# Kernel tuning notes

Hardware: AMD Instinct MI355X
Metric: run time of the kernel (lower is better)

The kernel has to match this reference:

```python
import jax, jax.numpy as jnp
import numpy as np

B, S, D = 4, 2048, 1024
NH, NKV = 16, 4
HD = D // NH  # 64


def _rope(x, freqs):
    # x: [B, H, S, HD], freqs: [B, S, HD//2]
    cos = jnp.concatenate([jnp.cos(freqs), jnp.cos(freqs)], axis=-1)[:, None]  # [B,1,S,HD]
    sin = jnp.concatenate([jnp.sin(freqs), jnp.sin(freqs)], axis=-1)[:, None]
    x1, x2 = x[..., : HD // 2], x[..., HD // 2:]
    rot = jnp.concatenate([-x2, x1], axis=-1)
    return x * cos + rot * sin


def setup_inputs() -> dict:
    key = jax.random.key(0)
    ks = jax.random.split(key, 9)
    return {
        "hidden_states": jax.random.normal(ks[0], (B, S, D), jnp.float32),
        "rotary_pos_emb": jax.random.normal(ks[1], (B, S, HD // 2), jnp.float32),
        "Wq": jax.random.normal(ks[2], (D, NH * HD), jnp.float32) * 0.02,
        "bq": jax.random.normal(ks[3], (NH * HD,), jnp.float32) * 0.02,
        "Wk": jax.random.normal(ks[4], (D, NKV * HD), jnp.float32) * 0.02,
        "bk": jax.random.normal(ks[5], (NKV * HD,), jnp.float32) * 0.02,
        "Wv": jax.random.normal(ks[6], (D, NKV * HD), jnp.float32) * 0.02,
        "bv": jax.random.normal(ks[7], (NKV * HD,), jnp.float32) * 0.02,
        "Wo": jax.random.normal(ks[8], (NH * HD, D), jnp.float32) * 0.02,
    }


def reference(hidden_states, rotary_pos_emb, Wq, bq, Wk, bk, Wv, bv, Wo):
    b, s, _ = hidden_states.shape
    # projections -> [B, H, S, HD]
    q = (hidden_states @ Wq + bq).reshape(b, s, NH, HD).transpose(0, 2, 1, 3)
    k = (hidden_states @ Wk + bk).reshape(b, s, NKV, HD).transpose(0, 2, 1, 3)
    v = (hidden_states @ Wv + bv).reshape(b, s, NKV, HD).transpose(0, 2, 1, 3)
    q = _rope(q, rotary_pos_emb)
    k = _rope(k, rotary_pos_emb)
    groups = NH // NKV
    k = jnp.repeat(k, groups, axis=1)  # [B, NH, S, HD]
    v = jnp.repeat(v, groups, axis=1)
    scaling = HD ** -0.5
    scores = jnp.einsum("bhqd,bhkd->bhqk", q, k) * scaling
    probs = jax.nn.softmax(scores.astype(jnp.float32), axis=-1).astype(q.dtype)
    out = jnp.einsum("bhqk,bhkd->bhqd", probs, v)
    out = out.transpose(0, 2, 1, 3).reshape(b, s, NH * HD)
    return out @ Wo
```

## Files before the change

kernel.cpp:

```cpp
#include <hip/hip_runtime.h>
#include <hip/hip_bf16.h>

#define BB 4
#define SS 2048
#define DD 1024
#define NH 16
#define NKV 4
#define HD 64
#define MROWS (BB*SS)
#define NQKV (NH*HD + 2*NKV*HD)
#define KOFF (NH*HD)

typedef short v8s __attribute__((ext_vector_type(8)));
typedef short v4s __attribute__((ext_vector_type(4)));
typedef float v4f __attribute__((ext_vector_type(4)));
typedef unsigned short u16;
typedef unsigned int u32;

__device__ __forceinline__ float bf2f(u16 u){
  union { float f; u32 i; } x; x.i = ((u32)u) << 16; return x.f;
}
__device__ __forceinline__ u16 f2bf(float f){
  union { __hip_bfloat16 h; u16 u; } x; x.h = __float2bfloat16(f); return x.u;
}
__device__ __forceinline__ u32 cvtpk(float lo, float hi){
  u32 r;
  asm("v_cvt_pk_bf16_f32 %0, %1, %2" : "=v"(r) : "v"(lo), "v"(hi));
  return r;
}
__device__ __forceinline__ float fmax3(float a, float b, float c){
  return fmaxf(fmaxf(a, b), c);
}
__device__ __forceinline__ void gl_lds16(const u16* g, u16* l){
  __builtin_amdgcn_global_load_lds(
      (const __attribute__((address_space(1))) u32*)g,
      (__attribute__((address_space(3))) u32*)l, 16, 0, 0);
}


__global__ void cast_x(const float* __restrict__ in, u16* __restrict__ out, int n4){
  int i = blockIdx.x*256 + threadIdx.x;
  if (i >= n4) return;
  float4 v = reinterpret_cast<const float4*>(in)[i];
  ushort4 o;
  o.x = f2bf(v.x); o.y = f2bf(v.y); o.z = f2bf(v.z); o.w = f2bf(v.w);
  reinterpret_cast<ushort4*>(out)[i] = o;
}

__global__ void build_bqkv(const float* __restrict__ Wq, const float* __restrict__ Wk,
                           const float* __restrict__ Wv, const float* __restrict__ bq,
                           const float* __restrict__ bk, const float* __restrict__ bv,
                           u16* __restrict__ Bt, float* __restrict__ bias){
  int idx = blockIdx.x*256 + threadIdx.x;
  int n = idx >> 10, k = idx & 1023;
  float v;
  if (n < 1024)      v = Wq[k*1024 + n];
  else if (n < 1280) v = Wk[k*256 + (n-1024)];
  else               v = Wv[k*256 + (n-1280)];
  Bt[idx] = f2bf(v);
  if (k == 0) bias[n] = (n < 1024) ? bq[n] : (n < 1280 ? bk[n-1024] : bv[n-1280]);
}

__global__ void build_wo(const float* __restrict__ Wo, u16* __restrict__ Bt){
  int idx = blockIdx.x*256 + threadIdx.x;
  int n = idx >> 10, k = idx & 1023;
  Bt[idx] = f2bf(Wo[k*1024 + n]);
}

__global__ void build_trig(const float* __restrict__ fr, float2* __restrict__ trig){
  int i = blockIdx.x*256 + threadIdx.x;
  float f = fr[i];
  float sn, cs; __sincosf(f, &sn, &cs);
  trig[i] = make_float2(cs, sn);
}

__global__ void rope_k(u16* __restrict__ QKV, const float* __restrict__ fr){
  int idx = blockIdx.x*256 + threadIdx.x;
  int d  = idx & 31;
  int hh = (idx >> 5) & 3;
  long row = idx >> 7;
  int col = KOFF + hh*HD + d;
  u16* p = QKV + row*NQKV;
  float x1 = bf2f(p[col]);
  float x2 = bf2f(p[col+32]);
  float f = fr[row*32 + d];
  float sn, cs; __sincosf(f, &sn, &cs);
  p[col]    = f2bf(x1*cs - x2*sn);
  p[col+32] = f2bf(x2*cs + x1*sn);
}


template<bool BIAS, typename OT>
__global__ __launch_bounds__(256) void gemm_bt(
    const u16* __restrict__ A, const u16* __restrict__ Bt,
    const float* __restrict__ bias, OT* __restrict__ C,
    int K, int ldc)
{
  __shared__ u16 As[128*32];
  __shared__ u16 Bs[128*32];
  const int tid = threadIdx.x;
  const int wid = tid >> 6, lane = tid & 63;
  const int g = lane >> 4, c = lane & 15;
  const long brow = (long)blockIdx.y * 128;
  const long bcol = (long)blockIdx.x * 128;
  const int wr = (wid >> 1) * 64, wc = (wid & 1) * 64;
  const int srow = tid >> 2;
  const int scol = (tid & 3) * 8;
  const u16* ga = &A [(brow + srow)*K + scol];
  const u16* gb = &Bt[(bcol + srow)*K + scol];
  u16* la = &As[(wid*64)*8];
  u16* lb = &Bs[(wid*64)*8];
  v4f acc[4][4] = {};
  for (int kt = 0; kt < K; kt += 32) {
    __syncthreads();
    gl_lds16(ga + kt,          la);
    gl_lds16(ga + 64*K + kt,   la + 256*8);
    gl_lds16(gb + kt,          lb);
    gl_lds16(gb + 64*K + kt,   lb + 256*8);
    __syncthreads();
    v8s af[4], bf[4];
    #pragma unroll
    for (int m=0;m<4;m++) af[m] = *reinterpret_cast<const v8s*>(&As[(wr + m*16 + c)*32 + g*8]);
    #pragma unroll
    for (int n=0;n<4;n++) bf[n] = *reinterpret_cast<const v8s*>(&Bs[(wc + n*16 + c)*32 + g*8]);
    __builtin_amdgcn_s_setprio(1);
    #pragma unroll
    for (int m=0;m<4;m++)
      #pragma unroll
      for (int n=0;n<4;n++)
        acc[m][n] = __builtin_amdgcn_mfma_f32_16x16x32_bf16(af[m], bf[n], acc[m][n], 0,0,0);
    __builtin_amdgcn_s_setprio(0);
  }
  #pragma unroll
  for (int m=0;m<4;m++)
    #pragma unroll
    for (int n=0;n<4;n++) {
      int col = (int)bcol + wc + n*16 + c;
      float badd = BIAS ? bias[col] : 0.0f;
      #pragma unroll
      for (int r2=0;r2<4;r2++){
        long row = brow + wr + m*16 + g*4 + r2;
        float v = acc[m][n][r2] + badd;
        if constexpr (sizeof(OT)==2) C[row*ldc + col] = (OT)f2bf(v);
        else                         C[row*ldc + col] = (OT)v;
      }
    }
}


__global__ __launch_bounds__(512) void attn_k(const u16* __restrict__ QKV,
                                              const float2* __restrict__ trig,
                                              u16* __restrict__ Out){
  __shared__ u16 Ks[2][64][72];
  __shared__ u16 Vs[2][64][72];
  const int tid = threadIdx.x;
  const int wid = tid >> 6, lane = tid & 63;
  const int g = lane >> 4, c = lane & 15;
  const int qt = blockIdx.x & 7;
  const int bh = blockIdx.x >> 3;
  const int b = bh >> 4, h = bh & 15;
  const int kvh = h >> 2;
  const u16* Qb = QKV + (long)b*SS*NQKV + h*HD;
  const u16* Kb = QKV + (long)b*SS*NQKV + KOFF + kvh*HD;
  const u16* Vb = Kb + NKV*HD;

  const float SCL = 0.125f * 1.44269504088896f;
  v8s qf[2][2];
  #pragma unroll
  for (int qn=0;qn<2;qn++){
    int lrow = qt*256 + wid*32 + qn*16 + c;
    v8s q0 = *reinterpret_cast<const v8s*>(&Qb[(long)lrow*NQKV + g*8]);
    v8s q1 = *reinterpret_cast<const v8s*>(&Qb[(long)lrow*NQKV + 32 + g*8]);
    const float4* tp = reinterpret_cast<const float4*>(
        trig + ((long)b*SS + lrow)*32 + g*8);
    float4 t0 = tp[0], t1 = tp[1], t2 = tp[2], t3 = tp[3];
    float cs_[8] = {t0.x,t0.z,t1.x,t1.z,t2.x,t2.z,t3.x,t3.z};
    float sn_[8] = {t0.y,t0.w,t1.y,t1.w,t2.y,t2.w,t3.y,t3.w};
    float r0[8], r1[8];
    #pragma unroll
    for (int j=0;j<8;j++){
      float x1 = bf2f((u16)q0[j]), x2 = bf2f((u16)q1[j]);
      r0[j] = (x1*cs_[j] - x2*sn_[j]) * SCL;
      r1[j] = (x2*cs_[j] + x1*sn_[j]) * SCL;
    }
    union { v8s v; u32 w[4]; } a0, a1;
    #pragma unroll
    for (int wi=0;wi<4;wi++){
      a0.w[wi] = cvtpk(r0[2*wi], r0[2*wi+1]);
      a1.w[wi] = cvtpk(r1[2*wi], r1[2*wi+1]);
    }
    qf[qn][0] = a0.v; qf[qn][1] = a1.v;
  }

  v8s onesf;
  {
    short ov = (c==0) ? (short)0x3F80 : (short)0;
    #pragma unroll
    for (int j=0;j<8;j++) onesf[j] = ov;
  }

  v4f o[2][5] = {};
  float mr[2] = {0.f, 0.f};

  const int krow = tid >> 3;
  const int kcol = (tid & 7) * 8;
  const int key0 = 2*(tid >> 4);
  const int dg4  = (tid & 15) * 4;
  const int slot0 = 32*(key0>>5) + 8*((key0>>2)&3) + 4*((key0>>4)&1) + (key0&3);
  int vofs[4];
  #pragma unroll
  for (int j=0;j<4;j++){
    int d = dg4 + j;
    int idx = (((slot0>>3) ^ (d>>3)) << 3) | (slot0 & 7);
    vofs[j] = d*72 + idx;
  }
  u16* VsF = &Vs[0][0][0];

  const u16* kp  = Kb + (long)krow*NQKV + kcol;
  const u16* vp0 = Vb + (long)key0*NQKV + dg4;
  const u16* vp1 = vp0 + NQKV;

  v8s kreg;
  union { v4s v; u32 w[2]; } vr0, vr1;

  {
    kreg  = *reinterpret_cast<const v8s*>(kp);
    vr0.v = *reinterpret_cast<const v4s*>(vp0);
    vr1.v = *reinterpret_cast<const v4s*>(vp1);
    *reinterpret_cast<v8s*>(&Ks[0][krow][kcol]) = kreg;
    #pragma unroll
    for (int j=0;j<4;j++){
      u32 pkd = __builtin_amdgcn_perm(vr1.w[j>>1], vr0.w[j>>1],
                                      (j&1) ? 0x07060302u : 0x05040100u);
      *reinterpret_cast<u32*>(&VsF[vofs[j]]) = pkd;
    }
  }
  __syncthreads();

  int p = 0;
  for (int t = 0; t < SS/64; ++t){
    if (t+1 < SS/64) {
      long off = (long)(t+1)*64*NQKV;
      kreg  = *reinterpret_cast<const v8s*>(kp  + off);
      vr0.v = *reinterpret_cast<const v4s*>(vp0 + off);
      vr1.v = *reinterpret_cast<const v4s*>(vp1 + off);
    }

    v4f st[4][2];
    #pragma unroll
    for (int qn=0;qn<2;qn++){
      v4f mi = {-mr[qn], -mr[qn], -mr[qn], -mr[qn]};
      #pragma unroll
      for (int km=0;km<4;km++) st[km][qn] = mi;
    }
    #pragma unroll
    for (int ks=0;ks<2;ks++){
      v8s kf[4];
      #pragma unroll
      for (int km=0;km<4;km++)
        kf[km] = *reinterpret_cast<const v8s*>(&Ks[p][km*16 + c][ks*32 + g*8]);
      __builtin_amdgcn_s_setprio(1);
      #pragma unroll
      for (int km=0;km<4;km++)
        #pragma unroll
        for (int qn=0;qn<2;qn++)
          st[km][qn] = __builtin_amdgcn_mfma_f32_16x16x32_bf16(kf[km], qf[qn][ks], st[km][qn], 0,0,0);
      __builtin_amdgcn_s_setprio(0);
    }

    float al[2];
    bool upd[2];
    #pragma unroll
    for (int qn=0;qn<2;qn++){
      float t0 = fmax3(st[0][qn][0], st[0][qn][1], st[0][qn][2]);
      float t1 = fmax3(st[0][qn][3], st[1][qn][0], st[1][qn][1]);
      float t2 = fmax3(st[1][qn][2], st[1][qn][3], st[2][qn][0]);
      float t3 = fmax3(st[2][qn][1], st[2][qn][2], st[2][qn][3]);
      float t4 = fmax3(st[3][qn][0], st[3][qn][1], st[3][qn][2]);
      float mx = fmaxf(fmax3(t0, t1, t2), fmax3(t3, t4, st[3][qn][3]));
      upd[qn] = !__all(mx <= 8.0f);
      al[qn] = 1.0f;
      if (upd[qn]) {
        mx = fmaxf(mx, __shfl_xor(mx, 16));
        mx = fmaxf(mx, __shfl_xor(mx, 32));
        float d = fmaxf(mx, 0.0f);
        al[qn] = __builtin_amdgcn_exp2f(-d);
        mr[qn] += d;
        #pragma unroll
        for (int km=0;km<4;km++)
          #pragma unroll
          for (int r2=0;r2<4;r2++)
            st[km][qn][r2] -= d;
      }
      #pragma unroll
      for (int km=0;km<4;km++)
        #pragma unroll
        for (int r2=0;r2<4;r2++)
          st[km][qn][r2] = __builtin_amdgcn_exp2f(st[km][qn][r2]);
    }

    v8s pa[2][2];
    #pragma unroll
    for (int qm=0;qm<2;qm++)
      #pragma unroll
      for (int ks=0;ks<2;ks++){
        union { v8s v; u32 w[4]; } u;
        u.w[0] = cvtpk(st[2*ks  ][qm][0], st[2*ks  ][qm][1]);
        u.w[1] = cvtpk(st[2*ks  ][qm][2], st[2*ks  ][qm][3]);
        u.w[2] = cvtpk(st[2*ks+1][qm][0], st[2*ks+1][qm][1]);
        u.w[3] = cvtpk(st[2*ks+1][qm][2], st[2*ks+1][qm][3]);
        pa[qm][ks] = u.v;
      }

    if (upd[0] | upd[1]) {
      #pragma unroll
      for (int qm=0;qm<2;qm++)
        #pragma unroll
        for (int r2=0;r2<4;r2++){
          float a = __shfl(al[qm], g*4 + r2);
          #pragma unroll
          for (int dn=0;dn<5;dn++) o[qm][dn][r2] *= a;
        }
    }

    #pragma unroll
    for (int ks=0;ks<2;ks++){
      __builtin_amdgcn_s_setprio(1);
      #pragma unroll
      for (int dn=0;dn<4;dn++){
        int d0 = dn*16 + c;
        v8s vf = *reinterpret_cast<const v8s*>(&Vs[p][d0][(((ks*4+g) ^ (d0>>3)) << 3)]);
        #pragma unroll
        for (int qm=0;qm<2;qm++)
          o[qm][dn] = __builtin_amdgcn_mfma_f32_16x16x32_bf16(pa[qm][ks], vf, o[qm][dn], 0,0,0);
      }
      #pragma unroll
      for (int qm=0;qm<2;qm++)
        o[qm][4] = __builtin_amdgcn_mfma_f32_16x16x32_bf16(pa[qm][ks], onesf, o[qm][4], 0,0,0);
      __builtin_amdgcn_s_setprio(0);
    }

    if (t+1 < SS/64) {
      *reinterpret_cast<v8s*>(&Ks[p^1][krow][kcol]) = kreg;
      const int bofs = (p^1) * (64*72);
      #pragma unroll
      for (int j=0;j<4;j++){
        u32 pkd = __builtin_amdgcn_perm(vr1.w[j>>1], vr0.w[j>>1],
                                        (j&1) ? 0x07060302u : 0x05040100u);
        *reinterpret_cast<u32*>(&VsF[bofs + vofs[j]]) = pkd;
      }
    }
    __syncthreads();
    p ^= 1;
  }

  #pragma unroll
  for (int qm=0;qm<2;qm++)
    #pragma unroll
    for (int r2=0;r2<4;r2++){
      float l = __shfl(o[qm][4][r2], lane & 48);
      float inv = 1.0f / l;
      long row = (long)b*SS + qt*256 + wid*32 + qm*16 + g*4 + r2;
      #pragma unroll
      for (int dn=0;dn<4;dn++)
        Out[row*DD + h*HD + dn*16 + c] = f2bf(o[qm][dn][r2] * inv);
    }
}


extern "C" void kernel_launch(void* const* d_in, const int* in_sizes, int n_in,
                              void* d_out, int out_size, void* d_ws, size_t ws_size,
                              hipStream_t stream)
{
  const float* hs = (const float*)d_in[0];
  const float* fr = (const float*)d_in[1];
  const float* Wq = (const float*)d_in[2];
  const float* bq = (const float*)d_in[3];
  const float* Wk = (const float*)d_in[4];
  const float* bk = (const float*)d_in[5];
  const float* Wv = (const float*)d_in[6];
  const float* bv = (const float*)d_in[7];
  const float* Wo = (const float*)d_in[8];
  float* out = (float*)d_out;
  char* ws = (char*)d_ws;

  u16*   Xb   = (u16*)(ws);
  u16*   Bqkv = (u16*)(ws + 16777216);
  u16*   WoT  = (u16*)(ws + 16777216 + 3145728);
  float* bias = (float*)(ws + 16777216 + 3145728 + 2097152);
  u16*   QKV  = (u16*)(ws + 22028288);
  u16*   AO   = (u16*)(ws + 22028288 + 25165824);
  float2* trig = (float2*)Bqkv;

  cast_x    <<<8192, 256, 0, stream>>>(hs, Xb, MROWS*DD/4);
  build_bqkv<<<6144, 256, 0, stream>>>(Wq, Wk, Wv, bq, bk, bv, Bqkv, bias);
  build_wo  <<<4096, 256, 0, stream>>>(Wo, WoT);
  gemm_bt<true,  u16>  <<<dim3(NQKV/128, MROWS/128), 256, 0, stream>>>(Xb, Bqkv, bias, QKV, DD, NQKV);
  build_trig<<<1024, 256, 0, stream>>>(fr, trig);
  rope_k    <<<MROWS*NKV*32/256, 256, 0, stream>>>(QKV, fr);
  attn_k    <<<BB*NH*(SS/256), 512, 0, stream>>>(QKV, trig, AO);
  gemm_bt<false, float><<<dim3(DD/128, MROWS/128), 256, 0, stream>>>(AO, WoT, nullptr, out, DD, DD);
}
```

Measured before the change: 180.2 us.

## Give each attention wave 64 query rows and sum softmax denominators in registers

The attention kernel now runs 4 waves of 256 threads, each owning 64 query rows instead of 32. Each K/V fragment read from LDS therefore feeds twice as many MFMAs, and each thread loads twice as much of the next K/V tile. The row-sum is now accumulated with VALU adds and cross-lane shuffles at the end, replacing the extra MFMA against a ones vector. The cost is higher register pressure (more accumulators and Q fragments) and fewer waves per block to hide latency.

```diff
diff --git a/kernel.cpp b/kernel.cpp
--- a/kernel.cpp
+++ b/kernel.cpp
@@ -28,8 +28,11 @@
   asm("v_cvt_pk_bf16_f32 %0, %1, %2" : "=v"(r) : "v"(lo), "v"(hi));
   return r;
 }
-__device__ __forceinline__ float fmax3(float a, float b, float c){
-  return fmaxf(fmaxf(a, b), c);
+__device__ __forceinline__ v4f vmax4(v4f a, v4f b){
+  v4f r;
+  #pragma unroll
+  for (int j=0;j<4;j++) r[j] = fmaxf(a[j], b[j]);
+  return r;
 }
 __device__ __forceinline__ void gl_lds16(const u16* g, u16* l){
   __builtin_amdgcn_global_load_lds(
@@ -148,7 +151,7 @@
 }
 
 
-__global__ __launch_bounds__(512) void attn_k(const u16* __restrict__ QKV,
+__global__ __launch_bounds__(256) void attn_k(const u16* __restrict__ QKV,
                                               const float2* __restrict__ trig,
                                               u16* __restrict__ Out){
   __shared__ u16 Ks[2][64][72];
@@ -165,10 +168,10 @@
   const u16* Vb = Kb + NKV*HD;
 
   const float SCL = 0.125f * 1.44269504088896f;
-  v8s qf[2][2];
-  #pragma unroll
-  for (int qn=0;qn<2;qn++){
-    int lrow = qt*256 + wid*32 + qn*16 + c;
+  v8s qf[4][2];
+  #pragma unroll
+  for (int qn=0;qn<4;qn++){
+    int lrow = qt*256 + wid*64 + qn*16 + c;
     v8s q0 = *reinterpret_cast<const v8s*>(&Qb[(long)lrow*NQKV + g*8]);
     v8s q1 = *reinterpret_cast<const v8s*>(&Qb[(long)lrow*NQKV + 32 + g*8]);
     const float4* tp = reinterpret_cast<const float4*>(
@@ -192,47 +195,38 @@
     qf[qn][0] = a0.v; qf[qn][1] = a1.v;
   }
 
-  v8s onesf;
+  v4f o[4][4] = {};
+  float mr[4] = {0.f, 0.f, 0.f, 0.f};
+  float lr[4] = {0.f, 0.f, 0.f, 0.f};
+
+  const int krow = tid >> 2;
+  const int kcol = (tid & 3) * 16;
+  const int key0 = 2*(tid >> 3);
+  const int dg   = tid & 7;
+  const int slot0 = 32*(key0>>5) + 8*((key0>>2)&3) + 4*((key0>>4)&1) + (key0&3);
+  const int idx0  = (((slot0>>3) ^ dg) << 3) | (slot0 & 7);
+  const int vbase = (dg*8)*72 + idx0;
+  u16* VsF = &Vs[0][0][0];
+
+  const u16* kp0 = Kb + (long)krow*NQKV + kcol;
+  const u16* vp0 = Vb + (long)key0*NQKV + dg*8;
+  const u16* vp1 = vp0 + NQKV;
+
+  v8s kreg0, kreg1;
+  union { v8s v; u32 w[4]; } vr0, vr1;
+
   {
-    short ov = (c==0) ? (short)0x3F80 : (short)0;
-    #pragma unroll
-    for (int j=0;j<8;j++) onesf[j] = ov;
-  }
-
-  v4f o[2][5] = {};
-  float mr[2] = {0.f, 0.f};
-
-  const int krow = tid >> 3;
-  const int kcol = (tid & 7) * 8;
-  const int key0 = 2*(tid >> 4);
-  const int dg4  = (tid & 15) * 4;
-  const int slot0 = 32*(key0>>5) + 8*((key0>>2)&3) + 4*((key0>>4)&1) + (key0&3);
-  int vofs[4];
-  #pragma unroll
-  for (int j=0;j<4;j++){
-    int d = dg4 + j;
-    int idx = (((slot0>>3) ^ (d>>3)) << 3) | (slot0 & 7);
-    vofs[j] = d*72 + idx;
-  }
-  u16* VsF = &Vs[0][0][0];
-
-  const u16* kp  = Kb + (long)krow*NQKV + kcol;
-  const u16* vp0 = Vb + (long)key0*NQKV + dg4;
-  const u16* vp1 = vp0 + NQKV;
-
-  v8s kreg;
-  union { v4s v; u32 w[2]; } vr0, vr1;
-
-  {
-    kreg  = *reinterpret_cast<const v8s*>(kp);
-    vr0.v = *reinterpret_cast<const v4s*>(vp0);
-    vr1.v = *reinterpret_cast<const v4s*>(vp1);
-    *reinterpret_cast<v8s*>(&Ks[0][krow][kcol]) = kreg;
-    #pragma unroll
-    for (int j=0;j<4;j++){
+    kreg0 = *reinterpret_cast<const v8s*>(kp0);
+    kreg1 = *reinterpret_cast<const v8s*>(kp0 + 8);
+    vr0.v = *reinterpret_cast<const v8s*>(vp0);
+    vr1.v = *reinterpret_cast<const v8s*>(vp1);
+    *reinterpret_cast<v8s*>(&Ks[0][krow][kcol])     = kreg0;
+    *reinterpret_cast<v8s*>(&Ks[0][krow][kcol + 8]) = kreg1;
+    #pragma unroll
+    for (int j=0;j<8;j++){
       u32 pkd = __builtin_amdgcn_perm(vr1.w[j>>1], vr0.w[j>>1],
                                       (j&1) ? 0x07060302u : 0x05040100u);
-      *reinterpret_cast<u32*>(&VsF[vofs[j]]) = pkd;
+      *reinterpret_cast<u32*>(&VsF[vbase + j*72]) = pkd;
     }
   }
   __syncthreads();
@@ -241,14 +235,15 @@
   for (int t = 0; t < SS/64; ++t){
     if (t+1 < SS/64) {
       long off = (long)(t+1)*64*NQKV;
-      kreg  = *reinterpret_cast<const v8s*>(kp  + off);
-      vr0.v = *reinterpret_cast<const v4s*>(vp0 + off);
-      vr1.v = *reinterpret_cast<const v4s*>(vp1 + off);
-    }
-
-    v4f st[4][2];
-    #pragma unroll
-    for (int qn=0;qn<2;qn++){
+      kreg0 = *reinterpret_cast<const v8s*>(kp0 + off);
+      kreg1 = *reinterpret_cast<const v8s*>(kp0 + off + 8);
+      vr0.v = *reinterpret_cast<const v8s*>(vp0 + off);
+      vr1.v = *reinterpret_cast<const v8s*>(vp1 + off);
+    }
+
+    v4f st[4][4];
+    #pragma unroll
+    for (int qn=0;qn<4;qn++){
       v4f mi = {-mr[qn], -mr[qn], -mr[qn], -mr[qn]};
       #pragma unroll
       for (int km=0;km<4;km++) st[km][qn] = mi;
@@ -263,21 +258,17 @@
       #pragma unroll
       for (int km=0;km<4;km++)
         #pragma unroll
-        for (int qn=0;qn<2;qn++)
+        for (int qn=0;qn<4;qn++)
           st[km][qn] = __builtin_amdgcn_mfma_f32_16x16x32_bf16(kf[km], qf[qn][ks], st[km][qn], 0,0,0);
       __builtin_amdgcn_s_setprio(0);
     }
 
-    float al[2];
-    bool upd[2];
-    #pragma unroll
-    for (int qn=0;qn<2;qn++){
-      float t0 = fmax3(st[0][qn][0], st[0][qn][1], st[0][qn][2]);
-      float t1 = fmax3(st[0][qn][3], st[1][qn][0], st[1][qn][1]);
-      float t2 = fmax3(st[1][qn][2], st[1][qn][3], st[2][qn][0]);
-      float t3 = fmax3(st[2][qn][1], st[2][qn][2], st[2][qn][3]);
-      float t4 = fmax3(st[3][qn][0], st[3][qn][1], st[3][qn][2]);
-      float mx = fmaxf(fmax3(t0, t1, t2), fmax3(t3, t4, st[3][qn][3]));
+    float al[4];
+    bool upd[4];
+    #pragma unroll
+    for (int qn=0;qn<4;qn++){
+      v4f m4 = vmax4(vmax4(st[0][qn], st[1][qn]), vmax4(st[2][qn], st[3][qn]));
+      float mx = fmaxf(fmaxf(m4[0], m4[1]), fmaxf(m4[2], m4[3]));
       upd[qn] = !__all(mx <= 8.0f);
       al[qn] = 1.0f;
       if (upd[qn]) {
@@ -286,6 +277,7 @@
         float d = fmaxf(mx, 0.0f);
         al[qn] = __builtin_amdgcn_exp2f(-d);
         mr[qn] += d;
+        lr[qn] *= al[qn];
         #pragma unroll
         for (int km=0;km<4;km++)
           #pragma unroll
@@ -297,11 +289,13 @@
         #pragma unroll
         for (int r2=0;r2<4;r2++)
           st[km][qn][r2] = __builtin_amdgcn_exp2f(st[km][qn][r2]);
-    }
-
-    v8s pa[2][2];
-    #pragma unroll
-    for (int qm=0;qm<2;qm++)
+      v4f s4 = (st[0][qn] + st[1][qn]) + (st[2][qn] + st[3][qn]);
+      lr[qn] += (s4[0] + s4[1]) + (s4[2] + s4[3]);
+    }
+
+    v8s pa[4][2];
+    #pragma unroll
+    for (int qm=0;qm<4;qm++)
       #pragma unroll
       for (int ks=0;ks<2;ks++){
         union { v8s v; u32 w[4]; } u;
@@ -312,14 +306,14 @@
         pa[qm][ks] = u.v;
       }
 
-    if (upd[0] | upd[1]) {
-      #pragma unroll
-      for (int qm=0;qm<2;qm++)
+    if (upd[0] | upd[1] | upd[2] | upd[3]) {
+      #pragma unroll
+      for (int qm=0;qm<4;qm++)
         #pragma unroll
         for (int r2=0;r2<4;r2++){
           float a = __shfl(al[qm], g*4 + r2);
           #pragma unroll
-          for (int dn=0;dn<5;dn++) o[qm][dn][r2] *= a;
+          for (int dn=0;dn<4;dn++) o[qm][dn][r2] *= a;
         }
     }
 
@@ -331,23 +325,21 @@
         int d0 = dn*16 + c;
         v8s vf = *reinterpret_cast<const v8s*>(&Vs[p][d0][(((ks*4+g) ^ (d0>>3)) << 3)]);
         #pragma unroll
-        for (int qm=0;qm<2;qm++)
+        for (int qm=0;qm<4;qm++)
           o[qm][dn] = __builtin_amdgcn_mfma_f32_16x16x32_bf16(pa[qm][ks], vf, o[qm][dn], 0,0,0);
       }
-      #pragma unroll
-      for (int qm=0;qm<2;qm++)
-        o[qm][4] = __builtin_amdgcn_mfma_f32_16x16x32_bf16(pa[qm][ks], onesf, o[qm][4], 0,0,0);
       __builtin_amdgcn_s_setprio(0);
     }
 
     if (t+1 < SS/64) {
-      *reinterpret_cast<v8s*>(&Ks[p^1][krow][kcol]) = kreg;
+      *reinterpret_cast<v8s*>(&Ks[p^1][krow][kcol])     = kreg0;
+      *reinterpret_cast<v8s*>(&Ks[p^1][krow][kcol + 8]) = kreg1;
       const int bofs = (p^1) * (64*72);
       #pragma unroll
-      for (int j=0;j<4;j++){
+      for (int j=0;j<8;j++){
         u32 pkd = __builtin_amdgcn_perm(vr1.w[j>>1], vr0.w[j>>1],
                                         (j&1) ? 0x07060302u : 0x05040100u);
-        *reinterpret_cast<u32*>(&VsF[bofs + vofs[j]]) = pkd;
+        *reinterpret_cast<u32*>(&VsF[bofs + vbase + j*72]) = pkd;
       }
     }
     __syncthreads();
@@ -355,12 +347,16 @@
   }
 
   #pragma unroll
-  for (int qm=0;qm<2;qm++)
+  for (int qm=0;qm<4;qm++){
+    lr[qm] += __shfl_xor(lr[qm], 16);
+    lr[qm] += __shfl_xor(lr[qm], 32);
+  }
+  #pragma unroll
+  for (int qm=0;qm<4;qm++)
     #pragma unroll
     for (int r2=0;r2<4;r2++){
-      float l = __shfl(o[qm][4][r2], lane & 48);
-      float inv = 1.0f / l;
-      long row = (long)b*SS + qt*256 + wid*32 + qm*16 + g*4 + r2;
+      float inv = 1.0f / __shfl(lr[qm], g*4 + r2);
+      long row = (long)b*SS + qt*256 + wid*64 + qm*16 + g*4 + r2;
       #pragma unroll
       for (int dn=0;dn<4;dn++)
         Out[row*DD + h*HD + dn*16 + c] = f2bf(o[qm][dn][r2] * inv);
@@ -398,6 +394,6 @@
   gemm_bt<true,  u16>  <<<dim3(NQKV/128, MROWS/128), 256, 0, stream>>>(Xb, Bqkv, bias, QKV, DD, NQKV);
   build_trig<<<1024, 256, 0, stream>>>(fr, trig);
   rope_k    <<<MROWS*NKV*32/256, 256, 0, stream>>>(QKV, fr);
-  attn_k    <<<BB*NH*(SS/256), 512, 0, stream>>>(QKV, trig, AO);
+  attn_k    <<<BB*NH*(SS/256), 256, 0, stream>>>(QKV, trig, AO);
   gemm_bt<false, float><<<dim3(DD/128, MROWS/128), 256, 0, stream>>>(AO, WoT, nullptr, out, DD, DD);
 }
```

After: 225.5 us. 25.1% more time.
